# Optimization experiments

Hardware: AMD Instinct MI355X
Metric: run time of the kernel (lower is better)

Reference implementation:

```python
import jax, jax.numpy as jnp
import numpy as np

B, C_TEXT, C, T, S, K = 4, 192, 768, 2048, 1024, 12


def setup_inputs() -> dict:
    key = jax.random.key(0)
    ks = jax.random.split(key, 6)
    return {
        "y": jax.random.normal(ks[0], (B, C, T), jnp.float32),
        "y_mask": jnp.ones((B, T), jnp.float32),
        "text": jax.random.normal(ks[1], (B, C_TEXT, S), jnp.float32),
        "text_mask": jnp.ones((B, S), jnp.float32),
        "ge": jax.random.normal(ks[2], (B, C, 1), jnp.float32),
        "W": jax.random.normal(ks[3], (K, C, C_TEXT), jnp.float32) * 0.05,
        "b": jax.random.normal(ks[4], (K, C), jnp.float32) * 0.01,
        "scale": jnp.ones((K,), jnp.float32),
    }


def reference(y, y_mask, text, text_mask, ge, W, b, scale):
    # 12 parallel 1x1-conv projections, batched: [K,B,C,S]
    tp = jnp.einsum('koc,bcs->kbos', W, text) + b[:, None, :, None]
    tp = tp * scale[:, None, None, None]
    tp = tp * text_mask[None, :, None, :]          # mask text positions
    # cross-attention scores for all 12 heads: [K,B,T,S]
    attn = jnp.einsum('bct,kbcs->kbts', y, tp)
    attn_mask = y_mask[:, :, None] * text_mask[:, None, :]   # [B,T,S]
    attn = attn * attn_mask[None] / jnp.sqrt(jnp.float32(C))
    attn = jax.nn.softmax(attn, axis=-1)
    # per-head context summed over heads: [B,C_text,T]... note context uses raw text (192 ch)
    context = jnp.einsum('kbts,bcs->bct', attn, text)        # sums over k and s
    # original adds 12 contexts of shape [B,192,T]; broadcast-add against y [B,768,T]
    # mirrors torch broadcasting only if channel dims match -> pad context to C via tile? No:
    # torch einsum 'bts,bcs->bct' with text [B,192,S] yields [B,192,T]; y is [B,768,T].
    # Faithful to the code as written, the add relies on matching channels, so we
    # project context into C by zero-padding is NOT in source; instead the source
    # implies context channels == y channels. We follow source semantics: contexts
    # are computed against raw text; to keep shapes consistent we broadcast via tiling
    context = jnp.tile(context, (1, C // C_TEXT, 1))
    out = y + context + ge
    return out
```

## Files before the change

### kernel.cpp

```cpp
#include <hip/hip_runtime.h>
#include <hip/hip_bf16.h>

#define BB 4
#define CC 768
#define CT 192
#define TT 2048
#define SS 1024
#define KK 12

typedef __attribute__((ext_vector_type(8))) short bfrag8;
typedef __attribute__((ext_vector_type(4))) float f32x4;


__device__ inline unsigned pk2(float a, float b) {
    __hip_bfloat162 h2;
    h2.x = __float2bfloat16(a);
    h2.y = __float2bfloat16(b);
    return *reinterpret_cast<unsigned*>(&h2);
}
__device__ inline float unpk_lo(unsigned u) { return __uint_as_float(u << 16); }
__device__ inline float unpk_hi(unsigned u) {
    return __uint_as_float(u & 0xffff0000u);
}

__global__ __launch_bounds__(256) void k_pack_all(
    const float* __restrict__ text, const float* __restrict__ W,
    const float* __restrict__ y, __hip_bfloat16* __restrict__ textS,
    __hip_bfloat16* __restrict__ textC, __hip_bfloat16* __restrict__ WP,
    __hip_bfloat16* __restrict__ yP) {
    __shared__ float tile[32][64];
    const int blk = blockIdx.x;
    const int tid = threadIdx.x;

    if (blk < 32) {
        const int b = blk >> 3;
        const float* tb = text + (size_t)b * CT * SS;
        const int base = tid + (blk & 7) * 256;
        for (int e = base; e < 64 * 6 * 512; e += 2048) {
            int jj = e & 7, l = (e >> 3) & 63, cc = (e >> 9) % 6, st = e / 3072;
            int ct = cc * 32 + ((l >> 4) << 3) + jj;
            int s = st * 16 + (l & 15);
            textS[(size_t)b * 196608 + e] =
                __float2bfloat16(tb[(size_t)ct * SS + s]);
        }
        for (int e = base; e < 12 * 32 * 512; e += 2048) {
            int jj = e & 7, l = (e >> 3) & 63, scg = (e >> 9) & 31,
                ctt = e / 16384;
            int ct = ctt * 16 + (l & 15);
            int s = scg * 32 + ((l >> 4) << 3) + jj;
            textC[(size_t)b * 196608 + e] =
                __float2bfloat16(tb[(size_t)ct * SS + s]);
        }
    } else if (blk < 128) {
        const int k = (blk - 32) >> 3;
        const float* wk = W + (size_t)k * CC * CT;
        const int base = tid + ((blk - 32) & 7) * 256;
        for (int e = base; e < 12 * 24 * 512; e += 2048) {
            int j = e & 7, l = (e >> 3) & 63, oc = (e >> 9) % 24, nt = e / 12288;
            int ct = nt * 16 + (l & 15);
            int o = oc * 32 + ((l >> 4) << 3) + j;
            WP[(size_t)k * 147456 + e] =
                __float2bfloat16(wk[(size_t)o * CT + ct]);
        }
    } else {
        const int idx = blk - 128;
        const int b = idx >> 5;
        const int tq = idx & 31;
        const int t0 = tq * 64;
        const float* yb_ = y + (size_t)b * CC * TT;
        const int w = tid >> 6, l = tid & 63;
        const int l15 = l & 15, lg = l >> 4;
        const int row0 = tid >> 4;
        const int c4 = tid & 15;

        for (int oc = 0; oc < 24; ++oc) {
#pragma unroll
            for (int h = 0; h < 2; ++h) {
                const int row = row0 + h * 16;
                const float4 v = *reinterpret_cast<const float4*>(
                    yb_ + (size_t)(oc * 32 + row) * TT + t0 + c4 * 4);
                *reinterpret_cast<float4*>(&tile[row][c4 * 4]) = v;
            }
            __syncthreads();
            union {
                bfrag8 v8;
                short u[8];
            } A;
#pragma unroll
            for (int j = 0; j < 8; ++j)
                A.u[j] = (short)__bfloat16_as_ushort(
                    __float2bfloat16(tile[lg * 8 + j][w * 16 + l15]));
            __hip_bfloat16* dst =
                yP + (((size_t)(b * 128 + tq * 4 + w) * 24 + oc) * 512) +
                (size_t)l * 8;
            *reinterpret_cast<bfrag8*>(dst) = A.v8;
            __syncthreads();
        }
    }
}

__global__ __launch_bounds__(256, 2) void k_yw_mfma(
    const __hip_bfloat16* __restrict__ yP, const __hip_bfloat16* __restrict__ WP,
    __hip_bfloat16* __restrict__ ywA) {
    const int i = blockIdx.x;
    const int x = i & 7, j = i >> 3;
    const int b = x & 3;
    const int k = j >> 4;
    const int tx = (j & 15) | ((x >> 2) << 4);
    const int kb = k * BB + b;

    const int tid = threadIdx.x;
    const int w = tid >> 6, l = tid & 63;
    const int l15 = l & 15, lg = l >> 4;
    const int ttg0 = tx * 4;
    const int nt0 = 3 * w;

    __shared__ float ot[4][16][197];

    const short* ypb = reinterpret_cast<const short*>(yP) +
                       (((size_t)b * 128 + ttg0) * 24) * 512 + (size_t)l * 8;
    const short* wp = reinterpret_cast<const short*>(WP) +
                      (size_t)k * 147456 + (size_t)l * 8;

    f32x4 acc[3][4];
#pragma unroll
    for (int n = 0; n < 3; ++n)
#pragma unroll
        for (int tg = 0; tg < 4; ++tg) acc[n][tg] = (f32x4){0.f, 0.f, 0.f, 0.f};

    for (int oc = 0; oc < 24; ++oc) {
        bfrag8 af[4];
#pragma unroll
        for (int tg = 0; tg < 4; ++tg)
            af[tg] =
                *reinterpret_cast<const bfrag8*>(ypb + (tg * 24 + oc) * 512);
#pragma unroll
        for (int n = 0; n < 3; ++n) {
            bfrag8 bf = *reinterpret_cast<const bfrag8*>(
                wp + ((nt0 + n) * 24 + oc) * 512);
#pragma unroll
            for (int tg = 0; tg < 4; ++tg)
                acc[n][tg] = __builtin_amdgcn_mfma_f32_16x16x32_bf16(
                    af[tg], bf, acc[n][tg], 0, 0, 0);
        }
    }

#pragma unroll
    for (int n = 0; n < 3; ++n) {
        const int ct = (w * 3 + n) * 16 + l15;
#pragma unroll
        for (int tg = 0; tg < 4; ++tg)
#pragma unroll
            for (int r = 0; r < 4; ++r) ot[tg][lg * 4 + r][ct] = acc[n][tg][r];
    }
    __syncthreads();

    const size_t obase = ((size_t)kb * 128 + ttg0 + w) * 3072;
#pragma unroll
    for (int cc = 0; cc < 6; ++cc) {
        union {
            bfrag8 v8;
            short u[8];
        } A;
#pragma unroll
        for (int j2 = 0; j2 < 8; ++j2)
            A.u[j2] = (short)__bfloat16_as_ushort(
                __float2bfloat16(ot[w][l15][cc * 32 + lg * 8 + j2]));
        *reinterpret_cast<bfrag8*>(
            reinterpret_cast<short*>(ywA) + obase + cc * 512 + (size_t)l * 8) =
            A.v8;
    }
}

__global__ __launch_bounds__(256) void k_yb2(const float* __restrict__ y,
                                             const float* __restrict__ bias,
                                             float* __restrict__ yb) {
    const int b = blockIdx.y;
    const int t0 = blockIdx.x * 64;
    const int tid = threadIdx.x;
    const int tl = tid & 63, g = tid >> 6;

    __shared__ float bs[KK][CC];
    __shared__ float pb[4][64][KK];
    for (int i = tid; i < KK * CC; i += 256) bs[i / CC][i % CC] = bias[i];
    __syncthreads();

    float p[KK];
#pragma unroll
    for (int k = 0; k < KK; ++k) p[k] = 0.f;
    const float* yb_ = y + (size_t)b * CC * TT + t0 + tl;
    for (int o = g * 192; o < g * 192 + 192; ++o) {
        float v = yb_[(size_t)o * TT];
#pragma unroll
        for (int k = 0; k < KK; ++k) p[k] += v * bs[k][o];
    }
#pragma unroll
    for (int k = 0; k < KK; ++k) pb[g][tl][k] = p[k];
    __syncthreads();
    for (int i = tid; i < 64 * KK; i += 256) {
        int tt = i / KK, k = i % KK;
        float s = pb[0][tt][k] + pb[1][tt][k] + pb[2][tt][k] + pb[3][tt][k];
        yb[((size_t)k * BB + b) * TT + t0 + tt] = s;
    }
}

__global__ __launch_bounds__(512) void k_attn_fused(
    const float* __restrict__ ymask, const float* __restrict__ tmask,
    const float* __restrict__ scale, const __hip_bfloat16* __restrict__ ywA,
    const float* __restrict__ ybws, const __hip_bfloat16* __restrict__ textS,
    const __hip_bfloat16* __restrict__ textC, const float* __restrict__ y,
    const float* __restrict__ ge, float* __restrict__ out) {
    const int i = blockIdx.x;
    const int x = i & 7;
    const int b = x & 3;
    const int tt = (i >> 3) + ((x >> 2) << 6);
    const int t0 = tt * 16;
    const int tid = threadIdx.x;
    const int w = tid >> 6;
    const int l = tid & 63;
    const int l15 = l & 15, lg = l >> 4;
    const int ws0 = w * 128;

    __shared__ float lds_acc[8][8][64][4];
    __shared__ uint2 exp_buf[2][8][8][64];
    __shared__ float yb_s[KK][16];
    __shared__ float sc_s[KK];
    __shared__ __align__(16) float lred[2][2][16][8];

    if (tid < 192)
        yb_s[tid >> 4][tid & 15] =
            ybws[(size_t)((tid >> 4) * BB + b) * TT + t0 + (tid & 15)];
    if (tid < KK) sc_s[tid] = scale[tid];
    const f32x4 zero4 = (f32x4){0.f, 0.f, 0.f, 0.f};
#pragma unroll
    for (int st = 0; st < 8; ++st)
        *reinterpret_cast<f32x4*>(&lds_acc[w][st][l][0]) = zero4;
    __syncthreads();

    float tm2r[8];
#pragma unroll
    for (int st = 0; st < 8; ++st) {
        float m = tmask[b * SS + ws0 + st * 16 + l15];
        tm2r[st] = m * m;
    }
    float ymr[4];
#pragma unroll
    for (int r = 0; r < 4; ++r) ymr[r] = ymask[b * TT + t0 + lg * 4 + r];
    const float invs_l2e = 0.03608439182435161f * 1.4426950408889634f;

    const short* ywAs = reinterpret_cast<const short*>(ywA);
    const short* tS = reinterpret_cast<const short*>(textS);
    const short* tSw = tS + (((size_t)b * 64 + w * 8) * 6) * 512 + (size_t)l * 8;
    const size_t headStride = (size_t)BB * 128 * 3072;

    for (int kp = 0; kp < 6; ++kp) {
        bfrag8 af[2][6];
        const size_t ab0 =
            (((size_t)(2 * kp * BB + b) * 128 + tt) * 6) * 512 + (size_t)l * 8;
#pragma unroll
        for (int cc = 0; cc < 6; ++cc) {
            af[0][cc] = *reinterpret_cast<const bfrag8*>(ywAs + ab0 + cc * 512);
            af[1][cc] = *reinterpret_cast<const bfrag8*>(ywAs + ab0 +
                                                         headStride + cc * 512);
        }
        float cfr[2][4], ybk[2][4];
#pragma unroll
        for (int p = 0; p < 2; ++p) {
            const int k = 2 * kp + p;
            const float sk = sc_s[k] * invs_l2e;
#pragma unroll
            for (int r = 0; r < 4; ++r) {
                const float cf = sk * ymr[r];
                cfr[p][r] = cf;
                ybk[p][r] = yb_s[k][lg * 4 + r] * cf;
            }
        }

        bfrag8 bfc[6];
#pragma unroll
        for (int cc = 0; cc < 6; ++cc)
            bfc[cc] = *reinterpret_cast<const bfrag8*>(tSw + cc * 512);

        float lrow[2][4] = {{0.f, 0.f, 0.f, 0.f}, {0.f, 0.f, 0.f, 0.f}};
#pragma unroll
        for (int st = 0; st < 8; ++st) {
            f32x4 av0 = zero4, av1 = zero4;
            __builtin_amdgcn_s_setprio(1);
#pragma unroll
            for (int cc = 0; cc < 6; ++cc) {
                av0 = __builtin_amdgcn_mfma_f32_16x16x32_bf16(af[0][cc],
                                                              bfc[cc], av0, 0,
                                                              0, 0);
                av1 = __builtin_amdgcn_mfma_f32_16x16x32_bf16(af[1][cc],
                                                              bfc[cc], av1, 0,
                                                              0, 0);
            }
            __builtin_amdgcn_s_setprio(0);
            if (st < 7) {
#pragma unroll
                for (int cc = 0; cc < 6; ++cc)
                    bfc[cc] = *reinterpret_cast<const bfrag8*>(
                        tSw + ((st + 1) * 6 + cc) * 512);
            }
#pragma unroll
            for (int r = 0; r < 4; ++r) {
                float e0 =
                    exp2f((av0[r] * cfr[0][r] + ybk[0][r]) * tm2r[st]);
                float e1 =
                    exp2f((av1[r] * cfr[1][r] + ybk[1][r]) * tm2r[st]);
                av0[r] = e0;
                av1[r] = e1;
                lrow[0][r] += e0;
                lrow[1][r] += e1;
            }
            exp_buf[0][w][st][l] =
                make_uint2(pk2(av0[0], av0[1]), pk2(av0[2], av0[3]));
            exp_buf[1][w][st][l] =
                make_uint2(pk2(av1[0], av1[1]), pk2(av1[2], av1[3]));
        }

#pragma unroll
        for (int d = 1; d < 16; d <<= 1)
#pragma unroll
            for (int p = 0; p < 2; ++p)
#pragma unroll
                for (int r = 0; r < 4; ++r)
                    lrow[p][r] += __shfl_xor(lrow[p][r], d);
        if (l15 == 0) {
#pragma unroll
            for (int p = 0; p < 2; ++p)
#pragma unroll
                for (int r = 0; r < 4; ++r)
                    lred[kp & 1][p][lg * 4 + r][w] = lrow[p][r];
        }
        __syncthreads();
        float rl[2][4];
#pragma unroll
        for (int p = 0; p < 2; ++p)
#pragma unroll
            for (int r = 0; r < 4; ++r) {
                const float4 v0 = *reinterpret_cast<const float4*>(
                    &lred[kp & 1][p][lg * 4 + r][0]);
                const float4 v1 = *reinterpret_cast<const float4*>(
                    &lred[kp & 1][p][lg * 4 + r][4]);
                rl[p][r] = 1.0f / (v0.x + v0.y + v0.z + v0.w + v1.x + v1.y +
                                   v1.z + v1.w);
            }
#pragma unroll
        for (int st = 0; st < 8; ++st) {
            const uint2 e0 = exp_buf[0][w][st][l];
            const uint2 e1 = exp_buf[1][w][st][l];
            f32x4 cur = *reinterpret_cast<f32x4*>(&lds_acc[w][st][l][0]);
            cur[0] += unpk_lo(e0.x) * rl[0][0] + unpk_lo(e1.x) * rl[1][0];
            cur[1] += unpk_hi(e0.x) * rl[0][1] + unpk_hi(e1.x) * rl[1][1];
            cur[2] += unpk_lo(e0.y) * rl[0][2] + unpk_lo(e1.y) * rl[1][2];
            cur[3] += unpk_hi(e0.y) * rl[0][3] + unpk_hi(e1.y) * rl[1][3];
            *reinterpret_cast<f32x4*>(&lds_acc[w][st][l][0]) = cur;
        }
    }
    __builtin_amdgcn_s_waitcnt(0);

    const short* tC = reinterpret_cast<const short*>(textC);
    f32x4 cacc[12];
#pragma unroll
    for (int c = 0; c < 12; ++c) cacc[c] = (f32x4){0.f, 0.f, 0.f, 0.f};

#pragma unroll
    for (int sc = 0; sc < 4; ++sc) {
        const int scg = w * 4 + sc;
        union {
            bfrag8 v8;
            unsigned u[4];
        } A;
#pragma unroll
        for (int jp = 0; jp < 4; ++jp) {
            const int s0 = scg * 32 + lg * 8 + jp * 2;
            const int reg0 = s0 >> 7, st0 = (s0 >> 4) & 7;
            const int lo0 = (s0 & 15) | ((l15 >> 2) << 4);
            const int s1 = s0 + 1;
            const int lo1 = (s1 & 15) | ((l15 >> 2) << 4);
            const int ro = l15 & 3;
            float a = lds_acc[reg0][st0][lo0][ro];
            float bb2 = lds_acc[s1 >> 7][(s1 >> 4) & 7][lo1][ro];
            A.u[jp] = pk2(a, bb2);
        }
#pragma unroll
        for (int ctt = 0; ctt < 12; ++ctt) {
            bfrag8 bf = *reinterpret_cast<const bfrag8*>(
                tC + (((size_t)b * 12 + ctt) * 32 + scg) * 512 + (size_t)l * 8);
            cacc[ctt] = __builtin_amdgcn_mfma_f32_16x16x32_bf16(
                A.v8, bf, cacc[ctt], 0, 0, 0);
        }
    }
    __syncthreads();

    float(*part)[16][192] =
        reinterpret_cast<float(*)[16][192]>(&lds_acc[0][0][0][0]);
    if (w < 4) {
#pragma unroll
        for (int ctt = 0; ctt < 12; ++ctt)
#pragma unroll
            for (int r = 0; r < 4; ++r)
                part[w][lg * 4 + r][ctt * 16 + l15] = cacc[ctt][r];
    }
    __syncthreads();
    if (w >= 4) {
#pragma unroll
        for (int ctt = 0; ctt < 12; ++ctt)
#pragma unroll
            for (int r = 0; r < 4; ++r)
                part[w - 4][lg * 4 + r][ctt * 16 + l15] += cacc[ctt][r];
    }
    __syncthreads();

    const float* yb_ = y + (size_t)b * CC * TT;
    float* ob = out + (size_t)b * CC * TT;
    const float* geb = ge + b * CC;
    for (int c = tid; c < CC; c += 512) {
        const float gev = geb[c];
        const int cm = c % CT;
        const float4* ysrc =
            reinterpret_cast<const float4*>(yb_ + (size_t)c * TT + t0);
        float4* od = reinterpret_cast<float4*>(ob + (size_t)c * TT + t0);
#pragma unroll
        for (int i4 = 0; i4 < 4; ++i4) {
            float4 v = ysrc[i4];
            const int row = i4 * 4;
            v.x += part[0][row + 0][cm] + part[1][row + 0][cm] +
                   part[2][row + 0][cm] + part[3][row + 0][cm] + gev;
            v.y += part[0][row + 1][cm] + part[1][row + 1][cm] +
                   part[2][row + 1][cm] + part[3][row + 1][cm] + gev;
            v.z += part[0][row + 2][cm] + part[1][row + 2][cm] +
                   part[2][row + 2][cm] + part[3][row + 2][cm] + gev;
            v.w += part[0][row + 3][cm] + part[1][row + 3][cm] +
                   part[2][row + 3][cm] + part[3][row + 3][cm] + gev;
            od[i4] = v;
        }
    }
}

extern "C" void kernel_launch(void* const* d_in, const int* in_sizes, int n_in,
                              void* d_out, int out_size, void* d_ws,
                              size_t ws_size, hipStream_t stream) {
    const float* y      = (const float*)d_in[0];
    const float* ymask  = (const float*)d_in[1];
    const float* text   = (const float*)d_in[2];
    const float* tmask  = (const float*)d_in[3];
    const float* ge     = (const float*)d_in[4];
    const float* W      = (const float*)d_in[5];
    const float* bias   = (const float*)d_in[6];
    const float* scale  = (const float*)d_in[7];
    float* out = (float*)d_out;

    char* ws = (char*)d_ws;
    __hip_bfloat16* ywA   = (__hip_bfloat16*)ws;
    float*          ybws  = (float*)(ws + 37748736);
    __hip_bfloat16* textS = (__hip_bfloat16*)(ws + 38141952);
    __hip_bfloat16* textC = (__hip_bfloat16*)(ws + 39714816);
    __hip_bfloat16* yP    = (__hip_bfloat16*)(ws + 58064896);
    __hip_bfloat16* WP    = (__hip_bfloat16*)(ws + 70647808);

    k_pack_all<<<256, 256, 0, stream>>>(text, W, y, textS, textC, WP, yP);
    k_yb2<<<dim3(TT / 64, BB), 256, 0, stream>>>(y, bias, ybws);
    k_yw_mfma<<<1536, 256, 0, stream>>>(yP, WP, ywA);
    k_attn_fused<<<512, 512, 0, stream>>>(ymask, tmask, scale, ywA, ybws,
                                          textS, textC, y, ge, out);
}
```

Baseline: 245.6 us.

## Fold bias projection into pack kernel, prefetch yw fragments, register-accumulate attention

Moves the yb bias-projection work into extra blocks of the pack kernel, dropping one launch and letting it run alongside the packing. The yw MFMA loop is fully unrolled and double-buffers its A/B fragments so global loads overlap the matrix ops. The attention kernel now handles one head per iteration instead of two: it stages that head's ywA fragment in LDS and accumulates the normalized probabilities in registers instead of read-modify-writing LDS through a bf16 exp buffer. The trade-offs are higher register pressure, an extra barrier per head, and half the MFMA work per loop iteration.

```diff
diff --git a/kernel.cpp b/kernel.cpp
--- a/kernel.cpp
+++ b/kernel.cpp
@@ -18,17 +18,14 @@
     h2.y = __float2bfloat16(b);
     return *reinterpret_cast<unsigned*>(&h2);
 }
-__device__ inline float unpk_lo(unsigned u) { return __uint_as_float(u << 16); }
-__device__ inline float unpk_hi(unsigned u) {
-    return __uint_as_float(u & 0xffff0000u);
-}
 
 __global__ __launch_bounds__(256) void k_pack_all(
     const float* __restrict__ text, const float* __restrict__ W,
-    const float* __restrict__ y, __hip_bfloat16* __restrict__ textS,
-    __hip_bfloat16* __restrict__ textC, __hip_bfloat16* __restrict__ WP,
-    __hip_bfloat16* __restrict__ yP) {
-    __shared__ float tile[32][64];
+    const float* __restrict__ y, const float* __restrict__ bias,
+    __hip_bfloat16* __restrict__ textS, __hip_bfloat16* __restrict__ textC,
+    __hip_bfloat16* __restrict__ WP, __hip_bfloat16* __restrict__ yP,
+    float* __restrict__ ybws) {
+    __shared__ __align__(16) char pk_lds[49152];
     const int blk = blockIdx.x;
     const int tid = threadIdx.x;
 
@@ -62,7 +59,8 @@
             WP[(size_t)k * 147456 + e] =
                 __float2bfloat16(wk[(size_t)o * CT + ct]);
         }
-    } else {
+    } else if (blk < 256) {
+        float(*tile)[64] = reinterpret_cast<float(*)[64]>(pk_lds);
         const int idx = blk - 128;
         const int b = idx >> 5;
         const int tq = idx & 31;
@@ -96,6 +94,37 @@
             *reinterpret_cast<bfrag8*>(dst) = A.v8;
             __syncthreads();
         }
+    } else {
+        float(*bs)[CC] = reinterpret_cast<float(*)[CC]>(pk_lds);
+        float(*pb)[32][KK] =
+            reinterpret_cast<float(*)[32][KK]>(pk_lds + 36864);
+        const int idx = blk - 256;
+        const int b = idx >> 6;
+        const int t0 = (idx & 63) * 32;
+        const int tl = tid & 31, g = tid >> 5;
+
+        for (int i = tid; i < KK * CC; i += 256) bs[i / CC][i % CC] = bias[i];
+        __syncthreads();
+
+        float p[KK];
+#pragma unroll
+        for (int k = 0; k < KK; ++k) p[k] = 0.f;
+        const float* yb_ = y + (size_t)b * CC * TT + t0 + tl;
+        for (int o = g * 96; o < g * 96 + 96; ++o) {
+            float v = yb_[(size_t)o * TT];
+#pragma unroll
+            for (int k = 0; k < KK; ++k) p[k] += v * bs[k][o];
+        }
+#pragma unroll
+        for (int k = 0; k < KK; ++k) pb[g][tl][k] = p[k];
+        __syncthreads();
+        for (int i = tid; i < 32 * KK; i += 256) {
+            int t = i / KK, k = i % KK;
+            float s = 0.f;
+#pragma unroll
+            for (int gg = 0; gg < 8; ++gg) s += pb[gg][t][k];
+            ybws[((size_t)k * BB + b) * TT + t0 + t] = s;
+        }
     }
 }
 
@@ -128,21 +157,33 @@
 #pragma unroll
         for (int tg = 0; tg < 4; ++tg) acc[n][tg] = (f32x4){0.f, 0.f, 0.f, 0.f};
 
+    bfrag8 af[2][4], bf[2][3];
+#pragma unroll
+    for (int tg = 0; tg < 4; ++tg)
+        af[0][tg] = *reinterpret_cast<const bfrag8*>(ypb + (tg * 24) * 512);
+#pragma unroll
+    for (int n = 0; n < 3; ++n)
+        bf[0][n] = *reinterpret_cast<const bfrag8*>(wp + ((nt0 + n) * 24) * 512);
+
+#pragma unroll
     for (int oc = 0; oc < 24; ++oc) {
-        bfrag8 af[4];
-#pragma unroll
-        for (int tg = 0; tg < 4; ++tg)
-            af[tg] =
-                *reinterpret_cast<const bfrag8*>(ypb + (tg * 24 + oc) * 512);
-#pragma unroll
-        for (int n = 0; n < 3; ++n) {
-            bfrag8 bf = *reinterpret_cast<const bfrag8*>(
-                wp + ((nt0 + n) * 24 + oc) * 512);
+        const int cur = oc & 1, nxt = cur ^ 1;
+        if (oc < 23) {
+#pragma unroll
+            for (int tg = 0; tg < 4; ++tg)
+                af[nxt][tg] = *reinterpret_cast<const bfrag8*>(
+                    ypb + (tg * 24 + oc + 1) * 512);
+#pragma unroll
+            for (int n = 0; n < 3; ++n)
+                bf[nxt][n] = *reinterpret_cast<const bfrag8*>(
+                    wp + ((nt0 + n) * 24 + oc + 1) * 512);
+        }
+#pragma unroll
+        for (int n = 0; n < 3; ++n)
 #pragma unroll
             for (int tg = 0; tg < 4; ++tg)
                 acc[n][tg] = __builtin_amdgcn_mfma_f32_16x16x32_bf16(
-                    af[tg], bf, acc[n][tg], 0, 0, 0);
-        }
+                    af[cur][tg], bf[cur][n], acc[n][tg], 0, 0, 0);
     }
 
 #pragma unroll
@@ -169,38 +210,6 @@
         *reinterpret_cast<bfrag8*>(
             reinterpret_cast<short*>(ywA) + obase + cc * 512 + (size_t)l * 8) =
             A.v8;
-    }
-}
-
-__global__ __launch_bounds__(256) void k_yb2(const float* __restrict__ y,
-                                             const float* __restrict__ bias,
-                                             float* __restrict__ yb) {
-    const int b = blockIdx.y;
-    const int t0 = blockIdx.x * 64;
-    const int tid = threadIdx.x;
-    const int tl = tid & 63, g = tid >> 6;
-
-    __shared__ float bs[KK][CC];
-    __shared__ float pb[4][64][KK];
-    for (int i = tid; i < KK * CC; i += 256) bs[i / CC][i % CC] = bias[i];
-    __syncthreads();
-
-    float p[KK];
-#pragma unroll
-    for (int k = 0; k < KK; ++k) p[k] = 0.f;
-    const float* yb_ = y + (size_t)b * CC * TT + t0 + tl;
-    for (int o = g * 192; o < g * 192 + 192; ++o) {
-        float v = yb_[(size_t)o * TT];
-#pragma unroll
-        for (int k = 0; k < KK; ++k) p[k] += v * bs[k][o];
-    }
-#pragma unroll
-    for (int k = 0; k < KK; ++k) pb[g][tl][k] = p[k];
-    __syncthreads();
-    for (int i = tid; i < 64 * KK; i += 256) {
-        int tt = i / KK, k = i % KK;
-        float s = pb[0][tt][k] + pb[1][tt][k] + pb[2][tt][k] + pb[3][tt][k];
-        yb[((size_t)k * BB + b) * TT + t0 + tt] = s;
     }
 }
 
@@ -221,21 +230,19 @@
     const int l15 = l & 15, lg = l >> 4;
     const int ws0 = w * 128;
 
-    __shared__ float lds_acc[8][8][64][4];
-    __shared__ uint2 exp_buf[2][8][8][64];
+    __shared__ __align__(16) char lds_raw[65536];
+    short(*af_s)[64][8] = reinterpret_cast<short(*)[64][8]>(lds_raw);
+    float(*lds_acc)[8][64][4] = reinterpret_cast<float(*)[8][64][4]>(lds_raw);
+    float(*part)[16][192] = reinterpret_cast<float(*)[16][192]>(lds_raw);
+
     __shared__ float yb_s[KK][16];
     __shared__ float sc_s[KK];
-    __shared__ __align__(16) float lred[2][2][16][8];
+    __shared__ __align__(16) float lred[2][16][8];
 
     if (tid < 192)
         yb_s[tid >> 4][tid & 15] =
             ybws[(size_t)((tid >> 4) * BB + b) * TT + t0 + (tid & 15)];
     if (tid < KK) sc_s[tid] = scale[tid];
-    const f32x4 zero4 = (f32x4){0.f, 0.f, 0.f, 0.f};
-#pragma unroll
-    for (int st = 0; st < 8; ++st)
-        *reinterpret_cast<f32x4*>(&lds_acc[w][st][l][0]) = zero4;
-    __syncthreads();
 
     float tm2r[8];
 #pragma unroll
@@ -247,33 +254,33 @@
 #pragma unroll
     for (int r = 0; r < 4; ++r) ymr[r] = ymask[b * TT + t0 + lg * 4 + r];
     const float invs_l2e = 0.03608439182435161f * 1.4426950408889634f;
+    const f32x4 zero4 = (f32x4){0.f, 0.f, 0.f, 0.f};
+
+    f32x4 accsum[8];
+#pragma unroll
+    for (int st = 0; st < 8; ++st) accsum[st] = zero4;
 
     const short* ywAs = reinterpret_cast<const short*>(ywA);
     const short* tS = reinterpret_cast<const short*>(textS);
     const short* tSw = tS + (((size_t)b * 64 + w * 8) * 6) * 512 + (size_t)l * 8;
-    const size_t headStride = (size_t)BB * 128 * 3072;
-
-    for (int kp = 0; kp < 6; ++kp) {
-        bfrag8 af[2][6];
+
+    for (int k = 0; k < KK; ++k) {
         const size_t ab0 =
-            (((size_t)(2 * kp * BB + b) * 128 + tt) * 6) * 512 + (size_t)l * 8;
-#pragma unroll
-        for (int cc = 0; cc < 6; ++cc) {
-            af[0][cc] = *reinterpret_cast<const bfrag8*>(ywAs + ab0 + cc * 512);
-            af[1][cc] = *reinterpret_cast<const bfrag8*>(ywAs + ab0 +
-                                                         headStride + cc * 512);
-        }
-        float cfr[2][4], ybk[2][4];
-#pragma unroll
-        for (int p = 0; p < 2; ++p) {
-            const int k = 2 * kp + p;
-            const float sk = sc_s[k] * invs_l2e;
-#pragma unroll
-            for (int r = 0; r < 4; ++r) {
-                const float cf = sk * ymr[r];
-                cfr[p][r] = cf;
-                ybk[p][r] = yb_s[k][lg * 4 + r] * cf;
-            }
+            (((size_t)(k * BB + b) * 128 + tt) * 6) * 512;
+        if (tid < 384) {
+            const int cc2 = tid >> 6, l2 = tid & 63;
+            bfrag8 v = *reinterpret_cast<const bfrag8*>(ywAs + ab0 +
+                                                        cc2 * 512 + l2 * 8);
+            *reinterpret_cast<bfrag8*>(&af_s[cc2][l2][0]) = v;
+        }
+        __syncthreads();
+
+        const float sk = sc_s[k] * invs_l2e;
+        float cfr[4], ybk[4];
+#pragma unroll
+        for (int r = 0; r < 4; ++r) {
+            cfr[r] = sk * ymr[r];
+            ybk[r] = yb_s[k][lg * 4 + r] * cfr[r];
         }
 
         bfrag8 bfc[6];
@@ -281,19 +288,18 @@
         for (int cc = 0; cc < 6; ++cc)
             bfc[cc] = *reinterpret_cast<const bfrag8*>(tSw + cc * 512);
 
-        float lrow[2][4] = {{0.f, 0.f, 0.f, 0.f}, {0.f, 0.f, 0.f, 0.f}};
+        f32x4 accv[8];
+        float lrow[4] = {0.f, 0.f, 0.f, 0.f};
 #pragma unroll
         for (int st = 0; st < 8; ++st) {
-            f32x4 av0 = zero4, av1 = zero4;
+            f32x4 av = zero4;
             __builtin_amdgcn_s_setprio(1);
 #pragma unroll
             for (int cc = 0; cc < 6; ++cc) {
-                av0 = __builtin_amdgcn_mfma_f32_16x16x32_bf16(af[0][cc],
-                                                              bfc[cc], av0, 0,
-                                                              0, 0);
-                av1 = __builtin_amdgcn_mfma_f32_16x16x32_bf16(af[1][cc],
-                                                              bfc[cc], av1, 0,
-                                                              0, 0);
+                bfrag8 a0 =
+                    *reinterpret_cast<const bfrag8*>(&af_s[cc][l][0]);
+                av = __builtin_amdgcn_mfma_f32_16x16x32_bf16(a0, bfc[cc], av,
+                                                             0, 0, 0);
             }
             __builtin_amdgcn_s_setprio(0);
             if (st < 7) {
@@ -304,66 +310,47 @@
             }
 #pragma unroll
             for (int r = 0; r < 4; ++r) {
-                float e0 =
-                    exp2f((av0[r] * cfr[0][r] + ybk[0][r]) * tm2r[st]);
-                float e1 =
-                    exp2f((av1[r] * cfr[1][r] + ybk[1][r]) * tm2r[st]);
-                av0[r] = e0;
-                av1[r] = e1;
-                lrow[0][r] += e0;
-                lrow[1][r] += e1;
+                float e = exp2f((av[r] * cfr[r] + ybk[r]) * tm2r[st]);
+                av[r] = e;
+                lrow[r] += e;
             }
-            exp_buf[0][w][st][l] =
-                make_uint2(pk2(av0[0], av0[1]), pk2(av0[2], av0[3]));
-            exp_buf[1][w][st][l] =
-                make_uint2(pk2(av1[0], av1[1]), pk2(av1[2], av1[3]));
+            accv[st] = av;
         }
 
 #pragma unroll
         for (int d = 1; d < 16; d <<= 1)
 #pragma unroll
-            for (int p = 0; p < 2; ++p)
-#pragma unroll
-                for (int r = 0; r < 4; ++r)
-                    lrow[p][r] += __shfl_xor(lrow[p][r], d);
+            for (int r = 0; r < 4; ++r) lrow[r] += __shfl_xor(lrow[r], d);
         if (l15 == 0) {
 #pragma unroll
-            for (int p = 0; p < 2; ++p)
-#pragma unroll
-                for (int r = 0; r < 4; ++r)
-                    lred[kp & 1][p][lg * 4 + r][w] = lrow[p][r];
+            for (int r = 0; r < 4; ++r) lred[k & 1][lg * 4 + r][w] = lrow[r];
         }
         __syncthreads();
-        float rl[2][4];
-#pragma unroll
-        for (int p = 0; p < 2; ++p)
-#pragma unroll
-            for (int r = 0; r < 4; ++r) {
-                const float4 v0 = *reinterpret_cast<const float4*>(
-                    &lred[kp & 1][p][lg * 4 + r][0]);
-                const float4 v1 = *reinterpret_cast<const float4*>(
-                    &lred[kp & 1][p][lg * 4 + r][4]);
-                rl[p][r] = 1.0f / (v0.x + v0.y + v0.z + v0.w + v1.x + v1.y +
-                                   v1.z + v1.w);
-            }
-#pragma unroll
-        for (int st = 0; st < 8; ++st) {
-            const uint2 e0 = exp_buf[0][w][st][l];
-            const uint2 e1 = exp_buf[1][w][st][l];
-            f32x4 cur = *reinterpret_cast<f32x4*>(&lds_acc[w][st][l][0]);
-            cur[0] += unpk_lo(e0.x) * rl[0][0] + unpk_lo(e1.x) * rl[1][0];
-            cur[1] += unpk_hi(e0.x) * rl[0][1] + unpk_hi(e1.x) * rl[1][1];
-            cur[2] += unpk_lo(e0.y) * rl[0][2] + unpk_lo(e1.y) * rl[1][2];
-            cur[3] += unpk_hi(e0.y) * rl[0][3] + unpk_hi(e1.y) * rl[1][3];
-            *reinterpret_cast<f32x4*>(&lds_acc[w][st][l][0]) = cur;
-        }
-    }
+        float rl[4];
+#pragma unroll
+        for (int r = 0; r < 4; ++r) {
+            const float4 v0 =
+                *reinterpret_cast<const float4*>(&lred[k & 1][lg * 4 + r][0]);
+            const float4 v1 =
+                *reinterpret_cast<const float4*>(&lred[k & 1][lg * 4 + r][4]);
+            rl[r] = 1.0f /
+                    (v0.x + v0.y + v0.z + v0.w + v1.x + v1.y + v1.z + v1.w);
+        }
+#pragma unroll
+        for (int st = 0; st < 8; ++st)
+#pragma unroll
+            for (int r = 0; r < 4; ++r) accsum[st][r] += accv[st][r] * rl[r];
+    }
+
+#pragma unroll
+    for (int st = 0; st < 8; ++st)
+        *reinterpret_cast<f32x4*>(&lds_acc[w][st][l][0]) = accsum[st];
     __builtin_amdgcn_s_waitcnt(0);
 
     const short* tC = reinterpret_cast<const short*>(textC);
     f32x4 cacc[12];
 #pragma unroll
-    for (int c = 0; c < 12; ++c) cacc[c] = (f32x4){0.f, 0.f, 0.f, 0.f};
+    for (int c = 0; c < 12; ++c) cacc[c] = zero4;
 
 #pragma unroll
     for (int sc = 0; sc < 4; ++sc) {
@@ -394,8 +381,6 @@
     }
     __syncthreads();
 
-    float(*part)[16][192] =
-        reinterpret_cast<float(*)[16][192]>(&lds_acc[0][0][0][0]);
     if (w < 4) {
 #pragma unroll
         for (int ctt = 0; ctt < 12; ++ctt)
@@ -460,8 +445,8 @@
     __hip_bfloat16* yP    = (__hip_bfloat16*)(ws + 58064896);
     __hip_bfloat16* WP    = (__hip_bfloat16*)(ws + 70647808);
 
-    k_pack_all<<<256, 256, 0, stream>>>(text, W, y, textS, textC, WP, yP);
-    k_yb2<<<dim3(TT / 64, BB), 256, 0, stream>>>(y, bias, ybws);
+    k_pack_all<<<512, 256, 0, stream>>>(text, W, y, bias, textS, textC, WP,
+                                        yP, ybws);
     k_yw_mfma<<<1536, 256, 0, stream>>>(yP, WP, ywA);
     k_attn_fused<<<512, 512, 0, stream>>>(ymask, tmask, scale, ywA, ybws,
                                           textS, textC, y, ge, out);
```

Result: no change. 247.8 us (+0.9%).
